# Kernel optimization log

Measured on AMD Instinct MI355X. Metric: run time of the kernel, lower is better.

Reference implementation:

```python
import jax, jax.numpy as jnp
import numpy as np

DIM = 768
NUM_HEADS = 12
HEAD_DIM = DIM // NUM_HEADS
SCALE = HEAD_DIM ** -0.5


def setup_inputs() -> dict:
    key = jax.random.key(0)
    ks = jax.random.split(key, 6)
    B, Lq, Lkv = 8, 1024, 1024
    return {
        "q": jax.random.normal(ks[0], (B, Lq, DIM), dtype=jnp.float32),
        "kv": jax.random.normal(ks[1], (B, Lkv, DIM), dtype=jnp.float32),
        "attn_pos": jax.random.normal(ks[2], (1, NUM_HEADS, Lq, Lkv), dtype=jnp.float32),
        "Wq": jax.random.normal(ks[3], (DIM, DIM), dtype=jnp.float32) * (DIM ** -0.5),
        "Wkv": jax.random.normal(ks[4], (2 * DIM, DIM), dtype=jnp.float32) * (DIM ** -0.5),
        "Wproj": jax.random.normal(ks[5], (DIM, DIM), dtype=jnp.float32) * (DIM ** -0.5),
        "bproj": jnp.zeros((DIM,), dtype=jnp.float32),
    }


def reference(q, kv, attn_pos, Wq, Wkv, Wproj, bproj):
    B, Lq, C = q.shape
    Lkv = kv.shape[1]
    H, D = NUM_HEADS, HEAD_DIM
    # q/kv projections (torch Linear: x @ W.T); attn_pos_encoding_only path
    qh = (q @ Wq.T).reshape(B, Lq, H, D).transpose(0, 2, 1, 3)        # (B,H,Lq,D)
    kvp = (kv @ Wkv.T).reshape(B, Lkv, 2, H, D).transpose(2, 0, 3, 1, 4)
    k, v = kvp[0], kvp[1]                                             # (B,H,Lkv,D)
    # scaled dot-product attention with additive positional bias
    attn = jnp.einsum('bhqd,bhkd->bhqk', qh, k) * SCALE + attn_pos    # (B,H,Lq,Lkv)
    attn = jax.nn.softmax(attn, axis=-1)
    x = jnp.einsum('bhqk,bhkd->bhqd', attn, v)                        # (B,H,Lq,D)
    x = x.transpose(0, 2, 1, 3).reshape(B, Lq, C)
    return x @ Wproj.T + bproj
```

## Files before the change

### kernel.cpp

```cpp
#include <hip/hip_runtime.h>

#define DIM 768
#define NHEADS 12
#define HDIM 64
#define BATCH 8
#define LQ 1024
#define LKV 1024
#define ATTN_SCALE 0.125f

typedef __bf16 bf16;
typedef __bf16 bf16x4 __attribute__((ext_vector_type(4)));
typedef __bf16 bf16x8 __attribute__((ext_vector_type(8)));
typedef short s16x4 __attribute__((ext_vector_type(4)));
typedef float f32x4 __attribute__((ext_vector_type(4)));

union B4 { bf16x4 h; s16x4 s; };

static __device__ __forceinline__ f32x4 mfma_k32(bf16x8 a, bf16x8 b, f32x4 c) {
    return __builtin_amdgcn_mfma_f32_16x16x32_bf16(a, b, c, 0, 0, 0);
}
static __device__ __forceinline__ f32x4 mfma_k16(s16x4 a, s16x4 b, f32x4 c) {
    return __builtin_amdgcn_mfma_f32_16x16x16bf16_1k(a, b, c, 0, 0, 0);
}

template<int OUT_F32, int A_BF16>
__global__ __launch_bounds__(256) void gemm_bt(
    const void* __restrict__ Ap, const float* __restrict__ B,
    void* __restrict__ Cp, const float* __restrict__ bias,
    int M, int N, int K)
{
    __shared__ bf16 As[128 * 40];
    __shared__ bf16 Bs[128 * 40];
    const int tid  = threadIdx.x;
    const int lane = tid & 63;
    const int wave = tid >> 6;
    const int wm = (wave >> 1) * 64;
    const int wn = (wave & 1) * 64;
    const int m0 = blockIdx.x * 128;
    const int n0 = blockIdx.y * 128;
    const int lq = lane & 15;
    const int quad = lane >> 4;
    const int row_l = tid >> 1;
    const int col_l = (tid & 1) * 16;

    f32x4 acc[4][4] = {};

    for (int k0 = 0; k0 < K; k0 += 32) {
        if (A_BF16) {
            const bf16* ga = (const bf16*)Ap + (size_t)(m0 + row_l) * K + k0 + col_l;
            *(uint4*)&As[row_l * 40 + col_l]     = *(const uint4*)(ga);
            *(uint4*)&As[row_l * 40 + col_l + 8] = *(const uint4*)(ga + 8);
        } else {
            const float* ga = (const float*)Ap + (size_t)(m0 + row_l) * K + k0 + col_l;
            float4 f0 = *(const float4*)(ga);
            float4 f1 = *(const float4*)(ga + 4);
            float4 f2 = *(const float4*)(ga + 8);
            float4 f3 = *(const float4*)(ga + 12);
            bf16x8 h0, h1;
            h0[0]=(bf16)f0.x; h0[1]=(bf16)f0.y; h0[2]=(bf16)f0.z; h0[3]=(bf16)f0.w;
            h0[4]=(bf16)f1.x; h0[5]=(bf16)f1.y; h0[6]=(bf16)f1.z; h0[7]=(bf16)f1.w;
            h1[0]=(bf16)f2.x; h1[1]=(bf16)f2.y; h1[2]=(bf16)f2.z; h1[3]=(bf16)f2.w;
            h1[4]=(bf16)f3.x; h1[5]=(bf16)f3.y; h1[6]=(bf16)f3.z; h1[7]=(bf16)f3.w;
            *(bf16x8*)&As[row_l * 40 + col_l]     = h0;
            *(bf16x8*)&As[row_l * 40 + col_l + 8] = h1;
        }
        {
            const float* gb = B + (size_t)(n0 + row_l) * K + k0 + col_l;
            float4 f0 = *(const float4*)(gb);
            float4 f1 = *(const float4*)(gb + 4);
            float4 f2 = *(const float4*)(gb + 8);
            float4 f3 = *(const float4*)(gb + 12);
            bf16x8 h0, h1;
            h0[0]=(bf16)f0.x; h0[1]=(bf16)f0.y; h0[2]=(bf16)f0.z; h0[3]=(bf16)f0.w;
            h0[4]=(bf16)f1.x; h0[5]=(bf16)f1.y; h0[6]=(bf16)f1.z; h0[7]=(bf16)f1.w;
            h1[0]=(bf16)f2.x; h1[1]=(bf16)f2.y; h1[2]=(bf16)f2.z; h1[3]=(bf16)f2.w;
            h1[4]=(bf16)f3.x; h1[5]=(bf16)f3.y; h1[6]=(bf16)f3.z; h1[7]=(bf16)f3.w;
            *(bf16x8*)&Bs[row_l * 40 + col_l]     = h0;
            *(bf16x8*)&Bs[row_l * 40 + col_l + 8] = h1;
        }
        __syncthreads();

        bf16x8 a[4], b[4];
        #pragma unroll
        for (int i = 0; i < 4; i++)
            a[i] = *(const bf16x8*)&As[(wm + i * 16 + lq) * 40 + quad * 8];
        #pragma unroll
        for (int j = 0; j < 4; j++)
            b[j] = *(const bf16x8*)&Bs[(wn + j * 16 + lq) * 40 + quad * 8];
        #pragma unroll
        for (int i = 0; i < 4; i++)
            #pragma unroll
            for (int j = 0; j < 4; j++)
                acc[i][j] = mfma_k32(a[i], b[j], acc[i][j]);
        __syncthreads();
    }

    #pragma unroll
    for (int i = 0; i < 4; i++) {
        #pragma unroll
        for (int j = 0; j < 4; j++) {
            #pragma unroll
            for (int r = 0; r < 4; r++) {
                int rr = m0 + wm + i * 16 + quad * 4 + r;
                int cc = n0 + wn + j * 16 + lq;
                if (OUT_F32) {
                    ((float*)Cp)[(size_t)rr * N + cc] = acc[i][j][r] + bias[cc];
                } else {
                    ((bf16*)Cp)[(size_t)rr * N + cc] = (bf16)acc[i][j][r];
                }
            }
        }
    }
}

__global__ __launch_bounds__(256) void transpose_v(const bf16* __restrict__ C2, bf16* __restrict__ Vt) {
    __shared__ bf16 T[64 * 72];
    int bh = blockIdx.x;
    int b = bh / NHEADS, h = bh % NHEADS;
    int kv0 = blockIdx.y * 64;
    int t = threadIdx.x;
    #pragma unroll
    for (int p = 0; p < 2; p++) {
        int row = (t >> 3) + p * 32;
        int c8  = (t & 7) * 8;
        const bf16* g = C2 + (size_t)(b * LKV + kv0 + row) * (2 * DIM) + DIM + h * HDIM + c8;
        *(uint4*)&T[row * 72 + c8] = *(const uint4*)g;
    }
    __syncthreads();
    #pragma unroll
    for (int p = 0; p < 2; p++) {
        int d  = (t >> 3) + p * 32;
        int l8 = (t & 7) * 8;
        bf16x8 tmp;
        #pragma unroll
        for (int j = 0; j < 8; j++) tmp[j] = T[(l8 + j) * 72 + d];
        bf16* o = Vt + ((size_t)(bh * HDIM + d)) * LKV + kv0 + l8;
        *(bf16x8*)o = tmp;
    }
}

__global__ __launch_bounds__(256) void attn_kernel(
    const bf16* __restrict__ C1,
    const bf16* __restrict__ C2,
    const bf16* __restrict__ Vt,
    const float* __restrict__ pos,
    bf16* __restrict__ O)
{
    __shared__ bf16 Qs[64 * 72];
    __shared__ bf16 Ks[64 * 72];
    __shared__ bf16 Vs[64 * 72];

    const int by = blockIdx.y;
    const int h = by >> 3, b = by & 7;
    const int bh = b * NHEADS + h;
    const int q0 = blockIdx.x * 64;
    const int t = threadIdx.x;
    const int lane = t & 63;
    const int w = t >> 6;
    const int lq = lane & 15;
    const int quad = lane >> 4;

    #pragma unroll
    for (int p = 0; p < 2; p++) {
        int row = (t >> 3) + p * 32;
        int c8  = (t & 7) * 8;
        const bf16* g = C1 + (size_t)(b * LQ + q0 + row) * DIM + h * HDIM + c8;
        *(uint4*)&Qs[row * 72 + c8] = *(const uint4*)g;
    }
    __syncthreads();
    bf16x8 qa[2];
    qa[0] = *(const bf16x8*)&Qs[(w * 16 + lq) * 72 +      quad * 8];
    qa[1] = *(const bf16x8*)&Qs[(w * 16 + lq) * 72 + 32 + quad * 8];
    __syncthreads();

    float m_r = -1e30f, l_r = 0.f;
    f32x4 o_acc[4] = {};

    const float4* pos4 = (const float4*)(pos + ((size_t)h * LQ + q0 + w * 16 + lq) * LKV);

    for (int kv0 = 0; kv0 < LKV; kv0 += 64) {
        #pragma unroll
        for (int p = 0; p < 2; p++) {
            int row = (t >> 3) + p * 32;
            int c8  = (t & 7) * 8;
            *(uint4*)&Ks[row * 72 + c8] =
                *(const uint4*)(C2 + (size_t)(b * LKV + kv0 + row) * (2 * DIM) + h * HDIM + c8);
            *(uint4*)&Vs[row * 72 + c8] =
                *(const uint4*)(Vt + (size_t)(bh * HDIM + row) * LKV + kv0 + c8);
        }
        __syncthreads();

        float4 pb[4];
        #pragma unroll
        for (int kvblk = 0; kvblk < 4; kvblk++)
            pb[kvblk] = pos4[(kv0 >> 2) + kvblk * 4 + quad];

        f32x4 s[4];
        #pragma unroll
        for (int kvblk = 0; kvblk < 4; kvblk++) {
            s[kvblk] = (f32x4){0.f, 0.f, 0.f, 0.f};
            #pragma unroll
            for (int kt = 0; kt < 2; kt++) {
                bf16x8 ak = *(const bf16x8*)&Ks[(kvblk * 16 + lq) * 72 + kt * 32 + quad * 8];
                s[kvblk] = mfma_k32(ak, qa[kt], s[kvblk]);
            }
        }

        float sv[4][4];
        #pragma unroll
        for (int kvblk = 0; kvblk < 4; kvblk++) {
            sv[kvblk][0] = s[kvblk][0] * ATTN_SCALE + pb[kvblk].x;
            sv[kvblk][1] = s[kvblk][1] * ATTN_SCALE + pb[kvblk].y;
            sv[kvblk][2] = s[kvblk][2] * ATTN_SCALE + pb[kvblk].z;
            sv[kvblk][3] = s[kvblk][3] * ATTN_SCALE + pb[kvblk].w;
        }

        float tmax = sv[0][0];
        #pragma unroll
        for (int kvblk = 0; kvblk < 4; kvblk++)
            #pragma unroll
            for (int r = 0; r < 4; r++)
                tmax = fmaxf(tmax, sv[kvblk][r]);
        tmax = fmaxf(tmax, __shfl_xor(tmax, 16));
        tmax = fmaxf(tmax, __shfl_xor(tmax, 32));
        float mn = fmaxf(m_r, tmax);
        float alpha = __expf(m_r - mn);
        float rs = 0.f;
        B4 pfrag[4];
        #pragma unroll
        for (int kvblk = 0; kvblk < 4; kvblk++) {
            #pragma unroll
            for (int r = 0; r < 4; r++) {
                float pv = __expf(sv[kvblk][r] - mn);
                rs += pv;
                pfrag[kvblk].h[r] = (bf16)pv;
            }
        }
        rs += __shfl_xor(rs, 16);
        rs += __shfl_xor(rs, 32);
        l_r = l_r * alpha + rs;
        m_r = mn;

        #pragma unroll
        for (int dblk = 0; dblk < 4; dblk++) {
            o_acc[dblk][0] *= alpha; o_acc[dblk][1] *= alpha;
            o_acc[dblk][2] *= alpha; o_acc[dblk][3] *= alpha;
        }

        #pragma unroll
        for (int dblk = 0; dblk < 4; dblk++) {
            #pragma unroll
            for (int kvblk = 0; kvblk < 4; kvblk++) {
                s16x4 va = *(const s16x4*)&Vs[(dblk * 16 + lq) * 72 + kvblk * 16 + quad * 4];
                o_acc[dblk] = mfma_k16(va, pfrag[kvblk].s, o_acc[dblk]);
            }
        }
        __syncthreads();
    }

    float inv = 1.f / l_r;
    const size_t orow = (size_t)(b * LQ + q0 + w * 16 + lq) * DIM + h * HDIM;
    #pragma unroll
    for (int dblk = 0; dblk < 4; dblk++) {
        B4 ob;
        #pragma unroll
        for (int r = 0; r < 4; r++) ob.h[r] = (bf16)(o_acc[dblk][r] * inv);
        *(s16x4*)&O[orow + dblk * 16 + quad * 4] = ob.s;
    }
}

extern "C" void kernel_launch(void* const* d_in, const int* in_sizes, int n_in,
                              void* d_out, int out_size, void* d_ws, size_t ws_size,
                              hipStream_t stream) {
    const float* q     = (const float*)d_in[0];
    const float* kv    = (const float*)d_in[1];
    const float* pos   = (const float*)d_in[2];
    const float* Wq    = (const float*)d_in[3];
    const float* Wkv   = (const float*)d_in[4];
    const float* Wproj = (const float*)d_in[5];
    const float* bproj = (const float*)d_in[6];
    float* out = (float*)d_out;

    char* ws = (char*)d_ws;
    size_t off = 0;
    auto alloc = [&](size_t bytes) -> void* {
        void* p = ws + off;
        off += (bytes + 255) & ~(size_t)255;
        return p;
    };

    const int M  = BATCH * LQ;
    bf16* C1   = (bf16*)alloc((size_t)M * DIM * 2);
    bf16* C2   = (bf16*)alloc((size_t)M * 2 * DIM * 2);
    bf16* Vt   = (bf16*)alloc((size_t)BATCH * NHEADS * HDIM * LKV * 2);
    bf16* Ob   = (bf16*)alloc((size_t)M * DIM * 2);

    gemm_bt<0, 0><<<dim3(M / 128, DIM / 128), 256, 0, stream>>>(q, Wq, C1, nullptr, M, DIM, DIM);
    gemm_bt<0, 0><<<dim3(M / 128, (2 * DIM) / 128), 256, 0, stream>>>(kv, Wkv, C2, nullptr, M, 2 * DIM, DIM);
    transpose_v<<<dim3(BATCH * NHEADS, LKV / 64), 256, 0, stream>>>(C2, Vt);
    attn_kernel<<<dim3(LQ / 64, NHEADS * BATCH), 256, 0, stream>>>(C1, C2, Vt, pos, Ob);
    gemm_bt<1, 1><<<dim3(M / 128, DIM / 128), 256, 0, stream>>>(Ob, Wproj, out, bproj, M, DIM, DIM);
}
```

Before: 331.7 us.

## Preconvert inputs to bf16, fuse V transpose into GEMM, widen attention query tile

Adds separate kernels that convert activations and weights to bf16 once, so the GEMMs load bf16 directly instead of converting fp32 on every tile load. The V projection GEMM now writes its output already transposed per head, removing the standalone transpose kernel. GEMM epilogues swap the MFMA operands so each lane can store four contiguous outputs at once. The attention kernel handles 128 queries per block, reusing each K/V tile for two query sub-tiles at the cost of more registers and an extra conversion pass over the inputs.

```diff
diff --git a/kernel.cpp b/kernel.cpp
--- a/kernel.cpp
+++ b/kernel.cpp
@@ -23,9 +23,38 @@
     return __builtin_amdgcn_mfma_f32_16x16x16bf16_1k(a, b, c, 0, 0, 0);
 }
 
-template<int OUT_F32, int A_BF16>
+__global__ void cvt_qkv(const float4* __restrict__ q, const float4* __restrict__ kv,
+                        bf16x4* __restrict__ qb, bf16x4* __restrict__ kvb, int n4) {
+    int i = blockIdx.x * 256 + threadIdx.x;
+    if (i >= n4) return;
+    const float4* src = blockIdx.y ? kv : q;
+    bf16x4* dst = blockIdx.y ? kvb : qb;
+    float4 v = src[i];
+    bf16x4 o;
+    o[0] = (bf16)v.x; o[1] = (bf16)v.y; o[2] = (bf16)v.z; o[3] = (bf16)v.w;
+    dst[i] = o;
+}
+
+__global__ void cvt_w(const float4* __restrict__ Wq, const float4* __restrict__ Wkv,
+                      const float4* __restrict__ Wp,
+                      bf16x4* __restrict__ wqb, bf16x4* __restrict__ wkvb,
+                      bf16x4* __restrict__ wpb, int n4) {
+    int i = blockIdx.x * 256 + threadIdx.x;
+    if (i >= n4) return;
+    int y = blockIdx.y;
+    const float4* src; bf16x4* dst;
+    if (y == 0)      { src = Wq;        dst = wqb; }
+    else if (y == 3) { src = Wp;        dst = wpb; }
+    else             { src = Wkv + (y - 1) * n4; dst = wkvb + (y - 1) * n4; }
+    float4 v = src[i];
+    bf16x4 o;
+    o[0] = (bf16)v.x; o[1] = (bf16)v.y; o[2] = (bf16)v.z; o[3] = (bf16)v.w;
+    dst[i] = o;
+}
+
+template<int MODE>
 __global__ __launch_bounds__(256) void gemm_bt(
-    const void* __restrict__ Ap, const float* __restrict__ B,
+    const bf16* __restrict__ A, const bf16* __restrict__ B,
     void* __restrict__ Cp, const float* __restrict__ bias,
     int M, int N, int K)
 {
@@ -33,9 +62,9 @@
     __shared__ bf16 Bs[128 * 40];
     const int tid  = threadIdx.x;
     const int lane = tid & 63;
-    const int wave = tid >> 6;
-    const int wm = (wave >> 1) * 64;
-    const int wn = (wave & 1) * 64;
+    const int w    = tid >> 6;
+    const int wm = (w >> 1) * 64;
+    const int wn = (w & 1) * 64;
     const int m0 = blockIdx.x * 128;
     const int n0 = blockIdx.y * 128;
     const int lq = lane & 15;
@@ -46,38 +75,12 @@
     f32x4 acc[4][4] = {};
 
     for (int k0 = 0; k0 < K; k0 += 32) {
-        if (A_BF16) {
-            const bf16* ga = (const bf16*)Ap + (size_t)(m0 + row_l) * K + k0 + col_l;
-            *(uint4*)&As[row_l * 40 + col_l]     = *(const uint4*)(ga);
-            *(uint4*)&As[row_l * 40 + col_l + 8] = *(const uint4*)(ga + 8);
-        } else {
-            const float* ga = (const float*)Ap + (size_t)(m0 + row_l) * K + k0 + col_l;
-            float4 f0 = *(const float4*)(ga);
-            float4 f1 = *(const float4*)(ga + 4);
-            float4 f2 = *(const float4*)(ga + 8);
-            float4 f3 = *(const float4*)(ga + 12);
-            bf16x8 h0, h1;
-            h0[0]=(bf16)f0.x; h0[1]=(bf16)f0.y; h0[2]=(bf16)f0.z; h0[3]=(bf16)f0.w;
-            h0[4]=(bf16)f1.x; h0[5]=(bf16)f1.y; h0[6]=(bf16)f1.z; h0[7]=(bf16)f1.w;
-            h1[0]=(bf16)f2.x; h1[1]=(bf16)f2.y; h1[2]=(bf16)f2.z; h1[3]=(bf16)f2.w;
-            h1[4]=(bf16)f3.x; h1[5]=(bf16)f3.y; h1[6]=(bf16)f3.z; h1[7]=(bf16)f3.w;
-            *(bf16x8*)&As[row_l * 40 + col_l]     = h0;
-            *(bf16x8*)&As[row_l * 40 + col_l + 8] = h1;
-        }
-        {
-            const float* gb = B + (size_t)(n0 + row_l) * K + k0 + col_l;
-            float4 f0 = *(const float4*)(gb);
-            float4 f1 = *(const float4*)(gb + 4);
-            float4 f2 = *(const float4*)(gb + 8);
-            float4 f3 = *(const float4*)(gb + 12);
-            bf16x8 h0, h1;
-            h0[0]=(bf16)f0.x; h0[1]=(bf16)f0.y; h0[2]=(bf16)f0.z; h0[3]=(bf16)f0.w;
-            h0[4]=(bf16)f1.x; h0[5]=(bf16)f1.y; h0[6]=(bf16)f1.z; h0[7]=(bf16)f1.w;
-            h1[0]=(bf16)f2.x; h1[1]=(bf16)f2.y; h1[2]=(bf16)f2.z; h1[3]=(bf16)f2.w;
-            h1[4]=(bf16)f3.x; h1[5]=(bf16)f3.y; h1[6]=(bf16)f3.z; h1[7]=(bf16)f3.w;
-            *(bf16x8*)&Bs[row_l * 40 + col_l]     = h0;
-            *(bf16x8*)&Bs[row_l * 40 + col_l + 8] = h1;
-        }
+        const bf16* ga = A + (size_t)(m0 + row_l) * K + k0 + col_l;
+        const bf16* gb = B + (size_t)(n0 + row_l) * K + k0 + col_l;
+        *(uint4*)&As[row_l * 40 + col_l]     = *(const uint4*)(ga);
+        *(uint4*)&As[row_l * 40 + col_l + 8] = *(const uint4*)(ga + 8);
+        *(uint4*)&Bs[row_l * 40 + col_l]     = *(const uint4*)(gb);
+        *(uint4*)&Bs[row_l * 40 + col_l + 8] = *(const uint4*)(gb + 8);
         __syncthreads();
 
         bf16x8 a[4], b[4];
@@ -91,69 +94,68 @@
         for (int i = 0; i < 4; i++)
             #pragma unroll
             for (int j = 0; j < 4; j++)
-                acc[i][j] = mfma_k32(a[i], b[j], acc[i][j]);
+                acc[i][j] = (MODE == 2) ? mfma_k32(a[i], b[j], acc[i][j])
+                                        : mfma_k32(b[j], a[i], acc[i][j]);
         __syncthreads();
     }
 
-    #pragma unroll
-    for (int i = 0; i < 4; i++) {
-        #pragma unroll
-        for (int j = 0; j < 4; j++) {
-            #pragma unroll
-            for (int r = 0; r < 4; r++) {
-                int rr = m0 + wm + i * 16 + quad * 4 + r;
-                int cc = n0 + wn + j * 16 + lq;
-                if (OUT_F32) {
-                    ((float*)Cp)[(size_t)rr * N + cc] = acc[i][j][r] + bias[cc];
+    if (MODE == 2) {
+        bf16* Vt = (bf16*)Cp;
+        #pragma unroll
+        for (int i = 0; i < 4; i++) {
+            const int base_m = m0 + wm + i * 16;
+            const int b_idx = base_m >> 10;
+            const int kvl = (base_m & 1023) + quad * 4;
+            #pragma unroll
+            for (int j = 0; j < 4; j++) {
+                const int nl = wn + j * 16 + lq;
+                const int h = (n0 + nl) >> 6;
+                const int d = (n0 + nl) & 63;
+                B4 pk;
+                #pragma unroll
+                for (int r = 0; r < 4; r++) pk.h[r] = (bf16)acc[i][j][r];
+                *(s16x4*)&Vt[(((size_t)b_idx * NHEADS + h) * HDIM + d) * LKV + kvl] = pk.s;
+            }
+        }
+    } else {
+        #pragma unroll
+        for (int i = 0; i < 4; i++) {
+            const size_t row = m0 + wm + i * 16 + lq;
+            #pragma unroll
+            for (int j = 0; j < 4; j++) {
+                const int col = n0 + wn + j * 16 + quad * 4;
+                if (MODE == 1) {
+                    float4 bj = *(const float4*)&bias[col];
+                    float4 o;
+                    o.x = acc[i][j][0] + bj.x; o.y = acc[i][j][1] + bj.y;
+                    o.z = acc[i][j][2] + bj.z; o.w = acc[i][j][3] + bj.w;
+                    *(float4*)&((float*)Cp)[row * N + col] = o;
                 } else {
-                    ((bf16*)Cp)[(size_t)rr * N + cc] = (bf16)acc[i][j][r];
+                    B4 pk;
+                    #pragma unroll
+                    for (int r = 0; r < 4; r++) pk.h[r] = (bf16)acc[i][j][r];
+                    *(s16x4*)&((bf16*)Cp)[row * N + col] = pk.s;
                 }
             }
         }
     }
 }
 
-__global__ __launch_bounds__(256) void transpose_v(const bf16* __restrict__ C2, bf16* __restrict__ Vt) {
-    __shared__ bf16 T[64 * 72];
-    int bh = blockIdx.x;
-    int b = bh / NHEADS, h = bh % NHEADS;
-    int kv0 = blockIdx.y * 64;
-    int t = threadIdx.x;
-    #pragma unroll
-    for (int p = 0; p < 2; p++) {
-        int row = (t >> 3) + p * 32;
-        int c8  = (t & 7) * 8;
-        const bf16* g = C2 + (size_t)(b * LKV + kv0 + row) * (2 * DIM) + DIM + h * HDIM + c8;
-        *(uint4*)&T[row * 72 + c8] = *(const uint4*)g;
-    }
-    __syncthreads();
-    #pragma unroll
-    for (int p = 0; p < 2; p++) {
-        int d  = (t >> 3) + p * 32;
-        int l8 = (t & 7) * 8;
-        bf16x8 tmp;
-        #pragma unroll
-        for (int j = 0; j < 8; j++) tmp[j] = T[(l8 + j) * 72 + d];
-        bf16* o = Vt + ((size_t)(bh * HDIM + d)) * LKV + kv0 + l8;
-        *(bf16x8*)o = tmp;
-    }
-}
-
 __global__ __launch_bounds__(256) void attn_kernel(
-    const bf16* __restrict__ C1,
-    const bf16* __restrict__ C2,
+    const bf16* __restrict__ Qb,
+    const bf16* __restrict__ Kb,
     const bf16* __restrict__ Vt,
     const float* __restrict__ pos,
     bf16* __restrict__ O)
 {
-    __shared__ bf16 Qs[64 * 72];
+    __shared__ bf16 Qs[128 * 72];
     __shared__ bf16 Ks[64 * 72];
     __shared__ bf16 Vs[64 * 72];
 
     const int by = blockIdx.y;
     const int h = by >> 3, b = by & 7;
     const int bh = b * NHEADS + h;
-    const int q0 = blockIdx.x * 64;
+    const int q0 = blockIdx.x * 128;
     const int t = threadIdx.x;
     const int lane = t & 63;
     const int w = t >> 6;
@@ -161,22 +163,27 @@
     const int quad = lane >> 4;
 
     #pragma unroll
-    for (int p = 0; p < 2; p++) {
+    for (int p = 0; p < 4; p++) {
         int row = (t >> 3) + p * 32;
         int c8  = (t & 7) * 8;
-        const bf16* g = C1 + (size_t)(b * LQ + q0 + row) * DIM + h * HDIM + c8;
-        *(uint4*)&Qs[row * 72 + c8] = *(const uint4*)g;
+        *(uint4*)&Qs[row * 72 + c8] =
+            *(const uint4*)(Qb + (size_t)(b * LQ + q0 + row) * DIM + h * HDIM + c8);
     }
     __syncthreads();
-    bf16x8 qa[2];
-    qa[0] = *(const bf16x8*)&Qs[(w * 16 + lq) * 72 +      quad * 8];
-    qa[1] = *(const bf16x8*)&Qs[(w * 16 + lq) * 72 + 32 + quad * 8];
-    __syncthreads();
-
-    float m_r = -1e30f, l_r = 0.f;
-    f32x4 o_acc[4] = {};
-
-    const float4* pos4 = (const float4*)(pos + ((size_t)h * LQ + q0 + w * 16 + lq) * LKV);
+    bf16x8 qa[2][2];
+    #pragma unroll
+    for (int s = 0; s < 2; s++) {
+        qa[s][0] = *(const bf16x8*)&Qs[(s * 64 + w * 16 + lq) * 72 +      quad * 8];
+        qa[s][1] = *(const bf16x8*)&Qs[(s * 64 + w * 16 + lq) * 72 + 32 + quad * 8];
+    }
+
+    float m_r[2] = {-1e30f, -1e30f}, l_r[2] = {0.f, 0.f};
+    f32x4 o_acc[2][4] = {};
+
+    const float4* pos4[2];
+    #pragma unroll
+    for (int s = 0; s < 2; s++)
+        pos4[s] = (const float4*)(pos + ((size_t)h * LQ + q0 + s * 64 + w * 16 + lq) * LKV);
 
     for (int kv0 = 0; kv0 < LKV; kv0 += 64) {
         #pragma unroll
@@ -184,88 +191,94 @@
             int row = (t >> 3) + p * 32;
             int c8  = (t & 7) * 8;
             *(uint4*)&Ks[row * 72 + c8] =
-                *(const uint4*)(C2 + (size_t)(b * LKV + kv0 + row) * (2 * DIM) + h * HDIM + c8);
+                *(const uint4*)(Kb + (size_t)(b * LKV + kv0 + row) * DIM + h * HDIM + c8);
             *(uint4*)&Vs[row * 72 + c8] =
                 *(const uint4*)(Vt + (size_t)(bh * HDIM + row) * LKV + kv0 + c8);
         }
         __syncthreads();
 
-        float4 pb[4];
-        #pragma unroll
-        for (int kvblk = 0; kvblk < 4; kvblk++)
-            pb[kvblk] = pos4[(kv0 >> 2) + kvblk * 4 + quad];
-
-        f32x4 s[4];
-        #pragma unroll
-        for (int kvblk = 0; kvblk < 4; kvblk++) {
-            s[kvblk] = (f32x4){0.f, 0.f, 0.f, 0.f};
-            #pragma unroll
-            for (int kt = 0; kt < 2; kt++) {
-                bf16x8 ak = *(const bf16x8*)&Ks[(kvblk * 16 + lq) * 72 + kt * 32 + quad * 8];
-                s[kvblk] = mfma_k32(ak, qa[kt], s[kvblk]);
-            }
-        }
-
-        float sv[4][4];
-        #pragma unroll
-        for (int kvblk = 0; kvblk < 4; kvblk++) {
-            sv[kvblk][0] = s[kvblk][0] * ATTN_SCALE + pb[kvblk].x;
-            sv[kvblk][1] = s[kvblk][1] * ATTN_SCALE + pb[kvblk].y;
-            sv[kvblk][2] = s[kvblk][2] * ATTN_SCALE + pb[kvblk].z;
-            sv[kvblk][3] = s[kvblk][3] * ATTN_SCALE + pb[kvblk].w;
-        }
-
-        float tmax = sv[0][0];
-        #pragma unroll
-        for (int kvblk = 0; kvblk < 4; kvblk++)
-            #pragma unroll
-            for (int r = 0; r < 4; r++)
-                tmax = fmaxf(tmax, sv[kvblk][r]);
-        tmax = fmaxf(tmax, __shfl_xor(tmax, 16));
-        tmax = fmaxf(tmax, __shfl_xor(tmax, 32));
-        float mn = fmaxf(m_r, tmax);
-        float alpha = __expf(m_r - mn);
-        float rs = 0.f;
-        B4 pfrag[4];
-        #pragma unroll
-        for (int kvblk = 0; kvblk < 4; kvblk++) {
-            #pragma unroll
-            for (int r = 0; r < 4; r++) {
-                float pv = __expf(sv[kvblk][r] - mn);
-                rs += pv;
-                pfrag[kvblk].h[r] = (bf16)pv;
-            }
-        }
-        rs += __shfl_xor(rs, 16);
-        rs += __shfl_xor(rs, 32);
-        l_r = l_r * alpha + rs;
-        m_r = mn;
-
+        #pragma unroll
+        for (int s = 0; s < 2; s++) {
+            float4 pb[4];
+            #pragma unroll
+            for (int kvblk = 0; kvblk < 4; kvblk++)
+                pb[kvblk] = pos4[s][(kv0 >> 2) + kvblk * 4 + quad];
+
+            f32x4 sc[4];
+            #pragma unroll
+            for (int kvblk = 0; kvblk < 4; kvblk++) {
+                sc[kvblk] = (f32x4){0.f, 0.f, 0.f, 0.f};
+                #pragma unroll
+                for (int kt = 0; kt < 2; kt++) {
+                    bf16x8 ak = *(const bf16x8*)&Ks[(kvblk * 16 + lq) * 72 + kt * 32 + quad * 8];
+                    sc[kvblk] = mfma_k32(ak, qa[s][kt], sc[kvblk]);
+                }
+            }
+
+            float sv[4][4];
+            #pragma unroll
+            for (int kvblk = 0; kvblk < 4; kvblk++) {
+                sv[kvblk][0] = sc[kvblk][0] * ATTN_SCALE + pb[kvblk].x;
+                sv[kvblk][1] = sc[kvblk][1] * ATTN_SCALE + pb[kvblk].y;
+                sv[kvblk][2] = sc[kvblk][2] * ATTN_SCALE + pb[kvblk].z;
+                sv[kvblk][3] = sc[kvblk][3] * ATTN_SCALE + pb[kvblk].w;
+            }
+
+            float tmax = sv[0][0];
+            #pragma unroll
+            for (int kvblk = 0; kvblk < 4; kvblk++)
+                #pragma unroll
+                for (int r = 0; r < 4; r++)
+                    tmax = fmaxf(tmax, sv[kvblk][r]);
+            tmax = fmaxf(tmax, __shfl_xor(tmax, 16));
+            tmax = fmaxf(tmax, __shfl_xor(tmax, 32));
+            float mn = fmaxf(m_r[s], tmax);
+            float alpha = __expf(m_r[s] - mn);
+            float rs = 0.f;
+            B4 pfrag[4];
+            #pragma unroll
+            for (int kvblk = 0; kvblk < 4; kvblk++) {
+                #pragma unroll
+                for (int r = 0; r < 4; r++) {
+                    float pv = __expf(sv[kvblk][r] - mn);
+                    rs += pv;
+                    pfrag[kvblk].h[r] = (bf16)pv;
+                }
+            }
+            rs += __shfl_xor(rs, 16);
+            rs += __shfl_xor(rs, 32);
+            l_r[s] = l_r[s] * alpha + rs;
+            m_r[s] = mn;
+
+            #pragma unroll
+            for (int dblk = 0; dblk < 4; dblk++) {
+                o_acc[s][dblk][0] *= alpha; o_acc[s][dblk][1] *= alpha;
+                o_acc[s][dblk][2] *= alpha; o_acc[s][dblk][3] *= alpha;
+            }
+
+            #pragma unroll
+            for (int dblk = 0; dblk < 4; dblk++) {
+                #pragma unroll
+                for (int kvblk = 0; kvblk < 4; kvblk++) {
+                    s16x4 va = *(const s16x4*)&Vs[(dblk * 16 + lq) * 72 + kvblk * 16 + quad * 4];
+                    o_acc[s][dblk] = mfma_k16(va, pfrag[kvblk].s, o_acc[s][dblk]);
+                }
+            }
+        }
+        __syncthreads();
+    }
+
+    #pragma unroll
+    for (int s = 0; s < 2; s++) {
+        float inv = 1.f / l_r[s];
+        const size_t orow = (size_t)(b * LQ + q0 + s * 64 + w * 16 + lq) * DIM + h * HDIM;
         #pragma unroll
         for (int dblk = 0; dblk < 4; dblk++) {
-            o_acc[dblk][0] *= alpha; o_acc[dblk][1] *= alpha;
-            o_acc[dblk][2] *= alpha; o_acc[dblk][3] *= alpha;
-        }
-
-        #pragma unroll
-        for (int dblk = 0; dblk < 4; dblk++) {
-            #pragma unroll
-            for (int kvblk = 0; kvblk < 4; kvblk++) {
-                s16x4 va = *(const s16x4*)&Vs[(dblk * 16 + lq) * 72 + kvblk * 16 + quad * 4];
-                o_acc[dblk] = mfma_k16(va, pfrag[kvblk].s, o_acc[dblk]);
-            }
-        }
-        __syncthreads();
-    }
-
-    float inv = 1.f / l_r;
-    const size_t orow = (size_t)(b * LQ + q0 + w * 16 + lq) * DIM + h * HDIM;
-    #pragma unroll
-    for (int dblk = 0; dblk < 4; dblk++) {
-        B4 ob;
-        #pragma unroll
-        for (int r = 0; r < 4; r++) ob.h[r] = (bf16)(o_acc[dblk][r] * inv);
-        *(s16x4*)&O[orow + dblk * 16 + quad * 4] = ob.s;
+            B4 ob;
+            #pragma unroll
+            for (int r = 0; r < 4; r++) ob.h[r] = (bf16)(o_acc[s][dblk][r] * inv);
+            *(s16x4*)&O[orow + dblk * 16 + quad * 4] = ob.s;
+        }
     }
 }
 
@@ -289,15 +302,30 @@
         return p;
     };
 
-    const int M  = BATCH * LQ;
-    bf16* C1   = (bf16*)alloc((size_t)M * DIM * 2);
-    bf16* C2   = (bf16*)alloc((size_t)M * 2 * DIM * 2);
+    const int M = BATCH * LQ;
+    bf16* qb   = (bf16*)alloc((size_t)M * DIM * 2);
+    bf16* kvb  = (bf16*)alloc((size_t)M * DIM * 2);
+    bf16* wqb  = (bf16*)alloc((size_t)DIM * DIM * 2);
+    bf16* wkvb = (bf16*)alloc((size_t)2 * DIM * DIM * 2);
+    bf16* wpb  = (bf16*)alloc((size_t)DIM * DIM * 2);
+    bf16* Qp   = (bf16*)alloc((size_t)M * DIM * 2);
+    bf16* Kp   = (bf16*)alloc((size_t)M * DIM * 2);
     bf16* Vt   = (bf16*)alloc((size_t)BATCH * NHEADS * HDIM * LKV * 2);
     bf16* Ob   = (bf16*)alloc((size_t)M * DIM * 2);
 
-    gemm_bt<0, 0><<<dim3(M / 128, DIM / 128), 256, 0, stream>>>(q, Wq, C1, nullptr, M, DIM, DIM);
-    gemm_bt<0, 0><<<dim3(M / 128, (2 * DIM) / 128), 256, 0, stream>>>(kv, Wkv, C2, nullptr, M, 2 * DIM, DIM);
-    transpose_v<<<dim3(BATCH * NHEADS, LKV / 64), 256, 0, stream>>>(C2, Vt);
-    attn_kernel<<<dim3(LQ / 64, NHEADS * BATCH), 256, 0, stream>>>(C1, C2, Vt, pos, Ob);
-    gemm_bt<1, 1><<<dim3(M / 128, DIM / 128), 256, 0, stream>>>(Ob, Wproj, out, bproj, M, DIM, DIM);
-}
+    {
+        int n4 = M * DIM / 4;
+        cvt_qkv<<<dim3((n4 + 255) / 256, 2), 256, 0, stream>>>(
+            (const float4*)q, (const float4*)kv, (bf16x4*)qb, (bf16x4*)kvb, n4);
+        int w4 = DIM * DIM / 4;
+        cvt_w<<<dim3((w4 + 255) / 256, 4), 256, 0, stream>>>(
+            (const float4*)Wq, (const float4*)Wkv, (const float4*)Wproj,
+            (bf16x4*)wqb, (bf16x4*)wkvb, (bf16x4*)wpb, w4);
+    }
+
+    gemm_bt<0><<<dim3(M / 128, DIM / 128), 256, 0, stream>>>(qb, wqb, Qp, nullptr, M, DIM, DIM);
+    gemm_bt<0><<<dim3(M / 128, DIM / 128), 256, 0, stream>>>(kvb, wkvb, Kp, nullptr, M, DIM, DIM);
+    gemm_bt<2><<<dim3(M / 128, DIM / 128), 256, 0, stream>>>(kvb, wkvb + (size_t)DIM * DIM, Vt, nullptr, M, DIM, DIM);
+    attn_kernel<<<dim3(LQ / 128, NHEADS * BATCH), 256, 0, stream>>>(Qp, Kp, Vt, pos, Ob);
+    gemm_bt<1><<<dim3(M / 128, DIM / 128), 256, 0, stream>>>(Ob, wpb, out, bproj, M, DIM, DIM);
+}
```

Result: slower. 345.2 us (+4.1%).
